# Kernel tuning notes

Measured on AMD Instinct MI355X. Metric: run time of the kernel, lower is better.

The kernel has to match this reference:

```python
import jax, jax.numpy as jnp
import numpy as np

B, S, L, F = 4, 4, 1024, 256
D, H = 256, 8
DH = D // H


def setup_inputs() -> dict:
    key = jax.random.key(0)
    ks = jax.random.split(key, 9)
    scale = 0.06  # ~1/sqrt(fan_in) init scale
    return {
        "x": jax.random.normal(ks[0], (B, S, L, F), dtype=jnp.float32),
        "Wq": jax.random.normal(ks[1], (D, F), dtype=jnp.float32) * scale,
        "bq": jnp.zeros((D,), dtype=jnp.float32),
        "Wk": jax.random.normal(ks[2], (D, F), dtype=jnp.float32) * scale,
        "bk": jnp.zeros((D,), dtype=jnp.float32),
        "Wv": jax.random.normal(ks[3], (D, F), dtype=jnp.float32) * scale,
        "bv": jnp.zeros((D,), dtype=jnp.float32),
        "Wo": jax.random.normal(ks[4], (D, D), dtype=jnp.float32) * scale,
        "bo": jnp.zeros((D,), dtype=jnp.float32),
    }


def reference(x, Wq, bq, Wk, bk, Wv, bv, Wo, bo):
    b, s, l, f = x.shape
    xr = x.reshape(b * s, l, f)  # [N, L, F] with N = batch*samples

    def split_heads(t):  # [N, L, D] -> [N, H, L, DH]
        return t.reshape(b * s, l, H, DH).transpose(0, 2, 1, 3)

    q = split_heads(xr @ Wq.T + bq)
    k = split_heads(xr @ Wk.T + bk)
    v = split_heads(xr @ Wv.T + bv)

    scores = jnp.einsum("nhqd,nhkd->nhqk", q, k) / jnp.sqrt(jnp.float32(DH))
    probs = jax.nn.softmax(scores, axis=-1)  # [N, H, L, L] — materialized as in original
    out = jnp.einsum("nhqk,nhkd->nhqd", probs, v)

    out = out.transpose(0, 2, 1, 3).reshape(b * s, l, D)
    out = out @ Wo.T + bo
    out = out.reshape(b, s, l, D)

    # softmax pooling over seq_len (dim=2)
    weight = jax.nn.softmax(out, axis=2)
    return jnp.sum(out * weight, axis=2)  # [B, S, D]
```

## Files before the change

kernel.cpp:

```cpp
#include <hip/hip_runtime.h>
#include <math.h>

#define N_SEQ 16
#define LEN   1024
#define FDIM  256
#define DDIM  256
#define NHEAD 8
#define DHD   32
#define ROWS  (N_SEQ * LEN)
#define QSCALE 0.17677669529663687f
#define QKVN  ((size_t)N_SEQ * NHEAD * LEN * DHD)

typedef __attribute__((ext_vector_type(8))) short bf16x8;
typedef __attribute__((ext_vector_type(4))) float f32x4;

__device__ __forceinline__ unsigned short f2bf(float f) {
    unsigned int u = __float_as_uint(f);
    unsigned int r = u + 0x7fffu + ((u >> 16) & 1u);
    return (unsigned short)(r >> 16);
}

__device__ __forceinline__ void load_lds16(const void* g, void* l) {
    __builtin_amdgcn_global_load_lds(
        (const __attribute__((address_space(1))) unsigned int*)g,
        (__attribute__((address_space(3))) unsigned int*)l, 16, 0, 0);
}

__global__ __launch_bounds__(256) void convert_bf16(
    const float* __restrict__ X,
    const float* __restrict__ Wq, const float* __restrict__ Wk,
    const float* __restrict__ Wv, const float* __restrict__ Wo,
    unsigned short* __restrict__ Xbf, unsigned short* __restrict__ Wbf)
{
    const size_t idx4 = ((size_t)blockIdx.x * 256 + threadIdx.x) * 4;
    const float* src;
    unsigned short* dst;
    if (idx4 < (size_t)ROWS * FDIM) {
        src = X + idx4;
        dst = Xbf + idx4;
    } else {
        const size_t wi = idx4 - (size_t)ROWS * FDIM;
        const int w = (int)(wi >> 16);
        const size_t off = wi & 65535;
        const float* Ws[4] = {Wq, Wk, Wv, Wo};
        src = Ws[w] + off;
        dst = Wbf + wi;
    }
    float4 v = *(const float4*)src;
    ushort4 u;
    u.x = f2bf(v.x); u.y = f2bf(v.y); u.z = f2bf(v.z); u.w = f2bf(v.w);
    *(ushort4*)dst = u;
}

template <int MODE>
__global__ __launch_bounds__(256) void gemm_bf16(
    const unsigned short* __restrict__ Ag, const unsigned short* __restrict__ Bg,
    const float* __restrict__ b0, const float* __restrict__ b1,
    const float* __restrict__ b2,
    unsigned short* __restrict__ OutB,
    float* __restrict__ pmO, float* __restrict__ plO, float* __restrict__ psO)
{
    __shared__ unsigned short As[16 * 512];
    __shared__ unsigned short Bs[16 * 512];

    const int m0 = blockIdx.x * 128;
    const int n0 = blockIdx.y * 128;
    const int tid  = threadIdx.x;
    const int wv   = tid >> 6;
    const int lane = tid & 63;
    const int l15  = lane & 15;
    const int quad = lane >> 4;
    const int wr = (wv & 1) * 64;
    const int wc = (wv >> 1) * 64;

    const int isB = wv >> 1;
    const unsigned short* __restrict__ Mg = isB ? Bg : Ag;
    const int mb0 = isB ? n0 : m0;
    unsigned short* Ms = isB ? Bs : As;
    const int fbase = (wv & 1) * 8;

    f32x4 acc[4][4] = {};

    for (int kt = 0; kt < 4; ++kt) {
        __syncthreads();
        #pragma unroll
        for (int f = 0; f < 8; ++f) {
            const int fi = fbase + f;
            const int i = fi >> 1, ks = fi & 1;
            load_lds16(Mg + (size_t)(mb0 + i*16 + l15) * 256 + kt*64 + ks*32 + quad*8,
                       Ms + fi * 512);
        }
        __syncthreads();
        #pragma unroll
        for (int ks = 0; ks < 2; ++ks) {
            bf16x8 af[4], bfr[4];
            #pragma unroll
            for (int i = 0; i < 4; ++i)
                af[i] = *(const bf16x8*)(&As[((((wv & 1)*4 + i)*2) + ks)*512 + lane*8]);
            #pragma unroll
            for (int j = 0; j < 4; ++j)
                bfr[j] = *(const bf16x8*)(&Bs[((((wv >> 1)*4 + j)*2) + ks)*512 + lane*8]);
            #pragma unroll
            for (int i = 0; i < 4; ++i)
                #pragma unroll
                for (int j = 0; j < 4; ++j)
                    acc[i][j] = __builtin_amdgcn_mfma_f32_16x16x32_bf16(
                        af[i], bfr[j], acc[i][j], 0, 0, 0);
        }
    }

    if (MODE == 0) {
        const int mat = n0 >> 8;
        const float scale = (mat == 0) ? QSCALE : 1.0f;
        const float* __restrict__ bias = (mat == 0) ? b0 : (mat == 1) ? b1 : b2;
        unsigned short* __restrict__ Out = OutB + (size_t)mat * QKVN;
        #pragma unroll
        for (int j = 0; j < 4; ++j) {
            const int c  = n0 + wc + j*16 + l15;
            const int cc = c & 255;
            const int h = cc >> 5, dh = cc & 31;
            const float bv = bias[cc];
            #pragma unroll
            for (int i = 0; i < 4; ++i)
                #pragma unroll
                for (int rr = 0; rr < 4; ++rr) {
                    const int r = m0 + wr + i*16 + quad*4 + rr;
                    const int n = r >> 10, l = r & 1023;
                    Out[(((size_t)(n*NHEAD + h)) * LEN + l) * DHD + dh] =
                        f2bf((acc[i][j][rr] + bv) * scale);
                }
        }
    } else {
        const int n    = blockIdx.x >> 3;
        const int tile = blockIdx.x & 7;
        __shared__ float red[4][64];

        float bv[4];
        #pragma unroll
        for (int j = 0; j < 4; ++j) bv[j] = b0[n0 + wc + j*16 + l15];
        #pragma unroll
        for (int i = 0; i < 4; ++i)
            #pragma unroll
            for (int j = 0; j < 4; ++j)
                #pragma unroll
                for (int rr = 0; rr < 4; ++rr)
                    acc[i][j][rr] += bv[j];

        float M[4];
        #pragma unroll
        for (int j = 0; j < 4; ++j) {
            float m = -1e30f;
            #pragma unroll
            for (int i = 0; i < 4; ++i)
                #pragma unroll
                for (int rr = 0; rr < 4; ++rr) m = fmaxf(m, acc[i][j][rr]);
            m = fmaxf(m, __shfl_xor(m, 16));
            m = fmaxf(m, __shfl_xor(m, 32));
            M[j] = m;
        }
        if (quad == 0) {
            #pragma unroll
            for (int j = 0; j < 4; ++j) red[wv][j*16 + l15] = M[j];
        }
        __syncthreads();
        #pragma unroll
        for (int j = 0; j < 4; ++j)
            M[j] = fmaxf(red[wv][j*16 + l15], red[wv^1][j*16 + l15]);
        __syncthreads();

        float LE[4], SE[4];
        #pragma unroll
        for (int j = 0; j < 4; ++j) {
            float le = 0.f, se = 0.f;
            #pragma unroll
            for (int i = 0; i < 4; ++i)
                #pragma unroll
                for (int rr = 0; rr < 4; ++rr) {
                    const float z = acc[i][j][rr];
                    const float e = __expf(z - M[j]);
                    le += e; se += z * e;
                }
            le += __shfl_xor(le, 16); le += __shfl_xor(le, 32);
            se += __shfl_xor(se, 16); se += __shfl_xor(se, 32);
            LE[j] = le; SE[j] = se;
        }
        if (quad == 0) {
            #pragma unroll
            for (int j = 0; j < 4; ++j) red[wv][j*16 + l15] = LE[j];
        }
        __syncthreads();
        float LEp[4];
        #pragma unroll
        for (int j = 0; j < 4; ++j) LEp[j] = red[wv^1][j*16 + l15];
        __syncthreads();
        if (quad == 0) {
            #pragma unroll
            for (int j = 0; j < 4; ++j) red[wv][j*16 + l15] = SE[j];
        }
        __syncthreads();
        float SEp[4];
        #pragma unroll
        for (int j = 0; j < 4; ++j) SEp[j] = red[wv^1][j*16 + l15];

        if ((wv & 1) == 0 && quad == 0) {
            #pragma unroll
            for (int j = 0; j < 4; ++j) {
                const int c = n0 + wc + j*16 + l15;
                const size_t o = ((size_t)n*8 + tile)*256 + c;
                pmO[o] = M[j];
                plO[o] = LE[j] + LEp[j];
                psO[o] = SE[j] + SEp[j];
            }
        }
    }
}

__global__ __launch_bounds__(256) void vtrans(
    const unsigned short* __restrict__ Vb, unsigned short* __restrict__ Vtb)
{
    __shared__ unsigned short Ls[64 * 34];

    const int nh = blockIdx.y;
    const int l0 = blockIdx.x * 64;
    const int tid = threadIdx.x;

    const int row = tid >> 2, c8 = (tid & 3) * 8;
    *(bf16x8*)(&Ls[row*34 + c8]) =
        *(const bf16x8*)(Vb + ((size_t)nh * LEN + l0 + row) * DHD + c8);
    __syncthreads();

    const int dh = tid >> 3, l8 = (tid & 7) * 8;
    ushort4 u0, u1;
    u0.x = Ls[(l8+0)*34 + dh]; u0.y = Ls[(l8+1)*34 + dh];
    u0.z = Ls[(l8+2)*34 + dh]; u0.w = Ls[(l8+3)*34 + dh];
    u1.x = Ls[(l8+4)*34 + dh]; u1.y = Ls[(l8+5)*34 + dh];
    u1.z = Ls[(l8+6)*34 + dh]; u1.w = Ls[(l8+7)*34 + dh];
    unsigned short* dst = Vtb + ((size_t)nh * DHD + dh) * LEN + l0 + l8;
    *(ushort4*)(dst)     = u0;
    *(ushort4*)(dst + 4) = u1;
}

#define LDK2 40
#define LDV2 136
#define LDPk 72
__global__ __launch_bounds__(256) void attn_mfma(
    const unsigned short* __restrict__ Qg_, const unsigned short* __restrict__ Kg_,
    const unsigned short* __restrict__ Vg_, unsigned short* __restrict__ Aout)
{
    __shared__ unsigned short Ks[128 * LDK2];
    __shared__ unsigned short Vs[32 * LDV2];
    __shared__ unsigned short Pb[4][16 * LDPk];

    const int nh = blockIdx.y;
    const int n  = nh >> 3, h = nh & 7;
    const int q0 = blockIdx.x * 64;
    const int tid  = threadIdx.x;
    const int wv   = tid >> 6;
    const int lane = tid & 63;
    const int l15  = lane & 15;
    const int quad = lane >> 4;

    const unsigned short* __restrict__ Qg = Qg_ + (size_t)nh * LEN * DHD;
    const unsigned short* __restrict__ Kg = Kg_ + (size_t)nh * LEN * DHD;
    const unsigned short* __restrict__ Vg = Vg_ + (size_t)nh * DHD * LEN;

    bf16x8 qf = *(const bf16x8*)(Qg + (size_t)(q0 + wv*16 + l15) * DHD + quad*8);

    f32x4 o0 = {0.f, 0.f, 0.f, 0.f};
    f32x4 o1 = {0.f, 0.f, 0.f, 0.f};
    float l_lane = 0.f;

    const int krow = tid >> 2, kc8 = (tid & 3) * 8;
    const int vrow = tid >> 3, vc8 = (tid & 7) * 8;

    unsigned short* __restrict__ Pw = &Pb[wv][0];

    for (int kt = 0; kt < LEN / 128; ++kt) {
        const int k0 = kt * 128;
        __syncthreads();
        *(bf16x8*)(&Ks[krow*LDK2 + kc8]) =
            *(const bf16x8*)(Kg + (size_t)(k0 + krow)*DHD + kc8);
        *(bf16x8*)(&Ks[(64 + krow)*LDK2 + kc8]) =
            *(const bf16x8*)(Kg + (size_t)(k0 + 64 + krow)*DHD + kc8);
        *(bf16x8*)(&Vs[vrow*LDV2 + vc8]) =
            *(const bf16x8*)(Vg + (size_t)vrow*LEN + k0 + vc8);
        *(bf16x8*)(&Vs[vrow*LDV2 + 64 + vc8]) =
            *(const bf16x8*)(Vg + (size_t)vrow*LEN + k0 + 64 + vc8);
        __syncthreads();

        #pragma unroll
        for (int half = 0; half < 2; ++half) {
            f32x4 st[4];
            #pragma unroll
            for (int sub = 0; sub < 4; ++sub) {
                bf16x8 kf = *(const bf16x8*)(&Ks[(half*64 + sub*16 + l15)*LDK2 + quad*8]);
                f32x4 z = {0.f, 0.f, 0.f, 0.f};
                st[sub] = __builtin_amdgcn_mfma_f32_16x16x32_bf16(kf, qf, z, 0, 0, 0);
            }
            #pragma unroll
            for (int sub = 0; sub < 4; ++sub) {
                const float p0 = __expf(st[sub][0]);
                const float p1 = __expf(st[sub][1]);
                const float p2 = __expf(st[sub][2]);
                const float p3 = __expf(st[sub][3]);
                l_lane += (p0 + p1) + (p2 + p3);
                uint2 pk;
                pk.x = (unsigned int)f2bf(p0) | ((unsigned int)f2bf(p1) << 16);
                pk.y = (unsigned int)f2bf(p2) | ((unsigned int)f2bf(p3) << 16);
                *(uint2*)(&Pw[l15*LDPk + sub*16 + quad*4]) = pk;
            }
            #pragma unroll
            for (int kk = 0; kk < 2; ++kk) {
                bf16x8 pf = *(const bf16x8*)(&Pw[l15*LDPk + kk*32 + quad*8]);
                bf16x8 va = *(const bf16x8*)(&Vs[l15*LDV2 + half*64 + kk*32 + quad*8]);
                bf16x8 vb = *(const bf16x8*)(&Vs[(16 + l15)*LDV2 + half*64 + kk*32 + quad*8]);
                o0 = __builtin_amdgcn_mfma_f32_16x16x32_bf16(va, pf, o0, 0, 0, 0);
                o1 = __builtin_amdgcn_mfma_f32_16x16x32_bf16(vb, pf, o1, 0, 0, 0);
            }
        }
    }

    l_lane += __shfl_xor(l_lane, 16);
    l_lane += __shfl_xor(l_lane, 32);
    const float linv = 1.f / l_lane;

    float* __restrict__ Tw = (float*)&Pb[wv][0];
    #pragma unroll
    for (int r = 0; r < 4; ++r) {
        Tw[l15*36 + quad*4 + r]      = o0[r] * linv;
        Tw[l15*36 + 16 + quad*4 + r] = o1[r] * linv;
    }
    __syncthreads();
    const int qr = lane >> 2, c8 = (lane & 3) * 8;
    float4 r0 = *(const float4*)(&Tw[qr*36 + c8]);
    float4 r1 = *(const float4*)(&Tw[qr*36 + c8 + 4]);
    unsigned short* dst = Aout + ((size_t)(n*LEN + q0 + wv*16 + qr)) * DDIM + h*DHD + c8;
    ushort4 u0, u1;
    u0.x = f2bf(r0.x); u0.y = f2bf(r0.y); u0.z = f2bf(r0.z); u0.w = f2bf(r0.w);
    u1.x = f2bf(r1.x); u1.y = f2bf(r1.y); u1.z = f2bf(r1.z); u1.w = f2bf(r1.w);
    *(ushort4*)(dst)     = u0;
    *(ushort4*)(dst + 4) = u1;
}

__global__ __launch_bounds__(256) void pool_merge(
    const float* __restrict__ pm, const float* __restrict__ pl,
    const float* __restrict__ ps, float* __restrict__ out)
{
    const int n = blockIdx.x;
    const int d = threadIdx.x;
    float M = -1e30f;
    #pragma unroll
    for (int t = 0; t < 8; ++t) M = fmaxf(M, pm[((size_t)n*8 + t)*256 + d]);
    float L = 0.f, S = 0.f;
    #pragma unroll
    for (int t = 0; t < 8; ++t) {
        const size_t idx = ((size_t)n*8 + t)*256 + d;
        const float w = __expf(pm[idx] - M);
        L += pl[idx] * w;
        S += ps[idx] * w;
    }
    out[n*256 + d] = S / L;
}

extern "C" void kernel_launch(void* const* d_in, const int* in_sizes, int n_in,
                              void* d_out, int out_size, void* d_ws, size_t ws_size,
                              hipStream_t stream)
{
    const float* x  = (const float*)d_in[0];
    const float* Wq = (const float*)d_in[1];
    const float* bq = (const float*)d_in[2];
    const float* Wk = (const float*)d_in[3];
    const float* bk = (const float*)d_in[4];
    const float* Wv = (const float*)d_in[5];
    const float* bv = (const float*)d_in[6];
    const float* Wo = (const float*)d_in[7];
    const float* bo = (const float*)d_in[8];
    float* out = (float*)d_out;

    char* base = (char*)d_ws;
    unsigned short* Xbf  = (unsigned short*)(base);
    unsigned short* Qb   = (unsigned short*)(base +  8388608);
    unsigned short* Kb   = (unsigned short*)(base + 16777216);
    unsigned short* Vb   = (unsigned short*)(base + 25165824);
    unsigned short* Vtb  = (unsigned short*)(base + 33554432);
    unsigned short* attnb= (unsigned short*)(base + 41943040);
    unsigned short* Wbf  = (unsigned short*)(base + 50331648);
    float* pm = (float*)(base + 50855936);
    float* pl = (float*)(base + 50987008);
    float* ps = (float*)(base + 51118080);
    const size_t need_bytes = 51249152;
    if (ws_size < need_bytes) return;

    convert_bf16<<<4352, 256, 0, stream>>>(x, Wq, Wk, Wv, Wo, Xbf, Wbf);
    gemm_bf16<0><<<dim3(ROWS/128, 6), 256, 0, stream>>>(
        Xbf, Wbf, bq, bk, bv, Qb, nullptr, nullptr, nullptr);
    vtrans<<<dim3(LEN/64, N_SEQ*NHEAD), 256, 0, stream>>>(Vb, Vtb);
    attn_mfma<<<dim3(LEN/64, N_SEQ*NHEAD), 256, 0, stream>>>(Qb, Kb, Vtb, attnb);
    gemm_bf16<1><<<dim3(ROWS/128, 2), 256, 0, stream>>>(
        attnb, Wbf + (size_t)768*256, bo, nullptr, nullptr, nullptr, pm, pl, ps);
    pool_merge<<<16, 256, 0, stream>>>(pm, pl, ps, out);
}
```

Baseline: 159.8 us.

## Write V in MFMA fragment layout, drop vtrans, stream K/V from registers

The QKV GEMM epilogue now writes V straight into the per-lane MFMA fragment layout, so the separate vtrans transpose kernel is removed. The attention kernel no longer stages K and V through shared memory with block barriers. Each lane loads its K/V fragments from global memory with one-step register prefetch, and each wave handles 64 queries (4 groups), so every K/V load is reused four times. P is now truncated to bf16 rather than rounded, and the row sum uses those same truncated values. This cuts launches and LDS traffic but raises register pressure and reduces the grid to a quarter as many blocks.

```diff
diff --git a/kernel.cpp b/kernel.cpp
--- a/kernel.cpp
+++ b/kernel.cpp
@@ -111,24 +111,52 @@
 
     if (MODE == 0) {
         const int mat = n0 >> 8;
-        const float scale = (mat == 0) ? QSCALE : 1.0f;
-        const float* __restrict__ bias = (mat == 0) ? b0 : (mat == 1) ? b1 : b2;
-        unsigned short* __restrict__ Out = OutB + (size_t)mat * QKVN;
-        #pragma unroll
-        for (int j = 0; j < 4; ++j) {
-            const int c  = n0 + wc + j*16 + l15;
-            const int cc = c & 255;
-            const int h = cc >> 5, dh = cc & 31;
-            const float bv = bias[cc];
-            #pragma unroll
-            for (int i = 0; i < 4; ++i)
-                #pragma unroll
-                for (int rr = 0; rr < 4; ++rr) {
-                    const int r = m0 + wr + i*16 + quad*4 + rr;
-                    const int n = r >> 10, l = r & 1023;
-                    Out[(((size_t)(n*NHEAD + h)) * LEN + l) * DHD + dh] =
-                        f2bf((acc[i][j][rr] + bv) * scale);
+        if (mat != 2) {
+            const float scale = (mat == 0) ? QSCALE : 1.0f;
+            const float* __restrict__ bias = (mat == 0) ? b0 : b1;
+            unsigned short* __restrict__ Out = OutB + (size_t)mat * QKVN;
+            #pragma unroll
+            for (int j = 0; j < 4; ++j) {
+                const int c  = n0 + wc + j*16 + l15;
+                const int cc = c & 255;
+                const int h = cc >> 5, dh = cc & 31;
+                const float bv = bias[cc];
+                #pragma unroll
+                for (int i = 0; i < 4; ++i)
+                    #pragma unroll
+                    for (int rr = 0; rr < 4; ++rr) {
+                        const int r = m0 + wr + i*16 + quad*4 + rr;
+                        const int n = r >> 10, l = r & 1023;
+                        Out[(((size_t)(n*NHEAD + h)) * LEN + l) * DHD + dh] =
+                            f2bf((acc[i][j][rr] + bv) * scale);
+                    }
+            }
+        } else {
+            unsigned short* __restrict__ Vf = OutB + 2 * QKVN;
+            #pragma unroll
+            for (int j = 0; j < 4; ++j) {
+                const int c  = n0 + wc + j*16 + l15;
+                const int cc = c & 255;
+                const int h = cc >> 5, dh = cc & 31;
+                const int dhb = dh >> 4, mv = dh & 15;
+                const float bv = b2[cc];
+                #pragma unroll
+                for (int i = 0; i < 4; ++i) {
+                    const int r0 = m0 + wr + i*16 + quad*4;
+                    const int n = r0 >> 10, l0 = r0 & 1023;
+                    const int nh = n*NHEAD + h;
+                    const int kb = l0 >> 5;
+                    const int qv = (l0 & 31) >> 3, jv0 = l0 & 7;
+                    const size_t addr =
+                        (((size_t)nh*32 + kb)*2 + dhb)*512 + (qv*16 + mv)*8 + jv0;
+                    ushort4 u;
+                    u.x = f2bf(acc[i][j][0] + bv);
+                    u.y = f2bf(acc[i][j][1] + bv);
+                    u.z = f2bf(acc[i][j][2] + bv);
+                    u.w = f2bf(acc[i][j][3] + bv);
+                    *(ushort4*)(Vf + addr) = u;
                 }
+            }
         }
     } else {
         const int n    = blockIdx.x >> 3;
@@ -215,45 +243,16 @@
     }
 }
 
-__global__ __launch_bounds__(256) void vtrans(
-    const unsigned short* __restrict__ Vb, unsigned short* __restrict__ Vtb)
-{
-    __shared__ unsigned short Ls[64 * 34];
-
-    const int nh = blockIdx.y;
-    const int l0 = blockIdx.x * 64;
-    const int tid = threadIdx.x;
-
-    const int row = tid >> 2, c8 = (tid & 3) * 8;
-    *(bf16x8*)(&Ls[row*34 + c8]) =
-        *(const bf16x8*)(Vb + ((size_t)nh * LEN + l0 + row) * DHD + c8);
-    __syncthreads();
-
-    const int dh = tid >> 3, l8 = (tid & 7) * 8;
-    ushort4 u0, u1;
-    u0.x = Ls[(l8+0)*34 + dh]; u0.y = Ls[(l8+1)*34 + dh];
-    u0.z = Ls[(l8+2)*34 + dh]; u0.w = Ls[(l8+3)*34 + dh];
-    u1.x = Ls[(l8+4)*34 + dh]; u1.y = Ls[(l8+5)*34 + dh];
-    u1.z = Ls[(l8+6)*34 + dh]; u1.w = Ls[(l8+7)*34 + dh];
-    unsigned short* dst = Vtb + ((size_t)nh * DHD + dh) * LEN + l0 + l8;
-    *(ushort4*)(dst)     = u0;
-    *(ushort4*)(dst + 4) = u1;
-}
-
-#define LDK2 40
-#define LDV2 136
 #define LDPk 72
 __global__ __launch_bounds__(256) void attn_mfma(
     const unsigned short* __restrict__ Qg_, const unsigned short* __restrict__ Kg_,
-    const unsigned short* __restrict__ Vg_, unsigned short* __restrict__ Aout)
+    const unsigned short* __restrict__ Vf_, unsigned short* __restrict__ Aout)
 {
-    __shared__ unsigned short Ks[128 * LDK2];
-    __shared__ unsigned short Vs[32 * LDV2];
     __shared__ unsigned short Pb[4][16 * LDPk];
 
     const int nh = blockIdx.y;
     const int n  = nh >> 3, h = nh & 7;
-    const int q0 = blockIdx.x * 64;
+    const int q0 = blockIdx.x * 256;
     const int tid  = threadIdx.x;
     const int wv   = tid >> 6;
     const int lane = tid & 63;
@@ -262,84 +261,104 @@
 
     const unsigned short* __restrict__ Qg = Qg_ + (size_t)nh * LEN * DHD;
     const unsigned short* __restrict__ Kg = Kg_ + (size_t)nh * LEN * DHD;
-    const unsigned short* __restrict__ Vg = Vg_ + (size_t)nh * DHD * LEN;
-
-    bf16x8 qf = *(const bf16x8*)(Qg + (size_t)(q0 + wv*16 + l15) * DHD + quad*8);
-
-    f32x4 o0 = {0.f, 0.f, 0.f, 0.f};
-    f32x4 o1 = {0.f, 0.f, 0.f, 0.f};
-    float l_lane = 0.f;
-
-    const int krow = tid >> 2, kc8 = (tid & 3) * 8;
-    const int vrow = tid >> 3, vc8 = (tid & 7) * 8;
+    const unsigned short* __restrict__ Vf = Vf_ + (size_t)nh * 32768;
+
+    bf16x8 qf[4];
+    #pragma unroll
+    for (int g = 0; g < 4; ++g)
+        qf[g] = *(const bf16x8*)(Qg + (size_t)(q0 + wv*64 + g*16 + l15) * DHD + quad*8);
+
+    f32x4 oA[4] = {{0.f,0.f,0.f,0.f},{0.f,0.f,0.f,0.f},{0.f,0.f,0.f,0.f},{0.f,0.f,0.f,0.f}};
+    f32x4 oB[4] = {{0.f,0.f,0.f,0.f},{0.f,0.f,0.f,0.f},{0.f,0.f,0.f,0.f},{0.f,0.f,0.f,0.f}};
+    float l_acc[4] = {0.f, 0.f, 0.f, 0.f};
+
+    const unsigned short* __restrict__ kbase = Kg + (size_t)l15 * DHD + quad*8;
+    const unsigned short* __restrict__ vbase = Vf + lane*8;
+
+    bf16x8 kf[4], vv[4];
+    #pragma unroll
+    for (int s = 0; s < 4; ++s) kf[s] = *(const bf16x8*)(kbase + (size_t)(s*16) * DHD);
+    #pragma unroll
+    for (int j = 0; j < 4; ++j) vv[j] = *(const bf16x8*)(vbase + j*512);
 
     unsigned short* __restrict__ Pw = &Pb[wv][0];
 
-    for (int kt = 0; kt < LEN / 128; ++kt) {
-        const int k0 = kt * 128;
-        __syncthreads();
-        *(bf16x8*)(&Ks[krow*LDK2 + kc8]) =
-            *(const bf16x8*)(Kg + (size_t)(k0 + krow)*DHD + kc8);
-        *(bf16x8*)(&Ks[(64 + krow)*LDK2 + kc8]) =
-            *(const bf16x8*)(Kg + (size_t)(k0 + 64 + krow)*DHD + kc8);
-        *(bf16x8*)(&Vs[vrow*LDV2 + vc8]) =
-            *(const bf16x8*)(Vg + (size_t)vrow*LEN + k0 + vc8);
-        *(bf16x8*)(&Vs[vrow*LDV2 + 64 + vc8]) =
-            *(const bf16x8*)(Vg + (size_t)vrow*LEN + k0 + 64 + vc8);
-        __syncthreads();
-
-        #pragma unroll
-        for (int half = 0; half < 2; ++half) {
+    for (int t = 0; t < 16; ++t) {
+        bf16x8 kn[4], vn[4];
+        if (t < 15) {
+            #pragma unroll
+            for (int s = 0; s < 4; ++s)
+                kn[s] = *(const bf16x8*)(kbase + (size_t)((t+1)*64 + s*16) * DHD);
+            #pragma unroll
+            for (int j = 0; j < 4; ++j)
+                vn[j] = *(const bf16x8*)(vbase + ((t+1)*4 + j)*512);
+        }
+        #pragma unroll
+        for (int g = 0; g < 4; ++g) {
             f32x4 st[4];
             #pragma unroll
-            for (int sub = 0; sub < 4; ++sub) {
-                bf16x8 kf = *(const bf16x8*)(&Ks[(half*64 + sub*16 + l15)*LDK2 + quad*8]);
+            for (int s = 0; s < 4; ++s) {
                 f32x4 z = {0.f, 0.f, 0.f, 0.f};
-                st[sub] = __builtin_amdgcn_mfma_f32_16x16x32_bf16(kf, qf, z, 0, 0, 0);
-            }
-            #pragma unroll
-            for (int sub = 0; sub < 4; ++sub) {
-                const float p0 = __expf(st[sub][0]);
-                const float p1 = __expf(st[sub][1]);
-                const float p2 = __expf(st[sub][2]);
-                const float p3 = __expf(st[sub][3]);
-                l_lane += (p0 + p1) + (p2 + p3);
+                st[s] = __builtin_amdgcn_mfma_f32_16x16x32_bf16(kf[s], qf[g], z, 0, 0, 0);
+            }
+            float lg = 0.f;
+            #pragma unroll
+            for (int s = 0; s < 4; ++s) {
+                const unsigned int a0 = __float_as_uint(__expf(st[s][0])) & 0xffff0000u;
+                const unsigned int a1 = __float_as_uint(__expf(st[s][1])) & 0xffff0000u;
+                const unsigned int a2 = __float_as_uint(__expf(st[s][2])) & 0xffff0000u;
+                const unsigned int a3 = __float_as_uint(__expf(st[s][3])) & 0xffff0000u;
+                lg += (__uint_as_float(a0) + __uint_as_float(a1))
+                    + (__uint_as_float(a2) + __uint_as_float(a3));
                 uint2 pk;
-                pk.x = (unsigned int)f2bf(p0) | ((unsigned int)f2bf(p1) << 16);
-                pk.y = (unsigned int)f2bf(p2) | ((unsigned int)f2bf(p3) << 16);
-                *(uint2*)(&Pw[l15*LDPk + sub*16 + quad*4]) = pk;
-            }
+                pk.x = (a0 >> 16) | a1;
+                pk.y = (a2 >> 16) | a3;
+                *(uint2*)(&Pw[l15*LDPk + s*16 + quad*4]) = pk;
+            }
+            l_acc[g] += lg;
             #pragma unroll
             for (int kk = 0; kk < 2; ++kk) {
                 bf16x8 pf = *(const bf16x8*)(&Pw[l15*LDPk + kk*32 + quad*8]);
-                bf16x8 va = *(const bf16x8*)(&Vs[l15*LDV2 + half*64 + kk*32 + quad*8]);
-                bf16x8 vb = *(const bf16x8*)(&Vs[(16 + l15)*LDV2 + half*64 + kk*32 + quad*8]);
-                o0 = __builtin_amdgcn_mfma_f32_16x16x32_bf16(va, pf, o0, 0, 0, 0);
-                o1 = __builtin_amdgcn_mfma_f32_16x16x32_bf16(vb, pf, o1, 0, 0, 0);
-            }
-        }
-    }
-
-    l_lane += __shfl_xor(l_lane, 16);
-    l_lane += __shfl_xor(l_lane, 32);
-    const float linv = 1.f / l_lane;
+                oA[g] = __builtin_amdgcn_mfma_f32_16x16x32_bf16(vv[kk*2+0], pf, oA[g], 0, 0, 0);
+                oB[g] = __builtin_amdgcn_mfma_f32_16x16x32_bf16(vv[kk*2+1], pf, oB[g], 0, 0, 0);
+            }
+        }
+        if (t < 15) {
+            #pragma unroll
+            for (int s = 0; s < 4; ++s) kf[s] = kn[s];
+            #pragma unroll
+            for (int j = 0; j < 4; ++j) vv[j] = vn[j];
+        }
+    }
+
+    float linv[4];
+    #pragma unroll
+    for (int g = 0; g < 4; ++g) {
+        float tsum = l_acc[g];
+        tsum += __shfl_xor(tsum, 16);
+        tsum += __shfl_xor(tsum, 32);
+        linv[g] = 1.f / tsum;
+    }
 
     float* __restrict__ Tw = (float*)&Pb[wv][0];
-    #pragma unroll
-    for (int r = 0; r < 4; ++r) {
-        Tw[l15*36 + quad*4 + r]      = o0[r] * linv;
-        Tw[l15*36 + 16 + quad*4 + r] = o1[r] * linv;
-    }
-    __syncthreads();
     const int qr = lane >> 2, c8 = (lane & 3) * 8;
-    float4 r0 = *(const float4*)(&Tw[qr*36 + c8]);
-    float4 r1 = *(const float4*)(&Tw[qr*36 + c8 + 4]);
-    unsigned short* dst = Aout + ((size_t)(n*LEN + q0 + wv*16 + qr)) * DDIM + h*DHD + c8;
-    ushort4 u0, u1;
-    u0.x = f2bf(r0.x); u0.y = f2bf(r0.y); u0.z = f2bf(r0.z); u0.w = f2bf(r0.w);
-    u1.x = f2bf(r1.x); u1.y = f2bf(r1.y); u1.z = f2bf(r1.z); u1.w = f2bf(r1.w);
-    *(ushort4*)(dst)     = u0;
-    *(ushort4*)(dst + 4) = u1;
+    #pragma unroll
+    for (int g = 0; g < 4; ++g) {
+        #pragma unroll
+        for (int r = 0; r < 4; ++r) {
+            Tw[l15*36 + quad*4 + r]      = oA[g][r] * linv[g];
+            Tw[l15*36 + 16 + quad*4 + r] = oB[g][r] * linv[g];
+        }
+        float4 r0 = *(const float4*)(&Tw[qr*36 + c8]);
+        float4 r1 = *(const float4*)(&Tw[qr*36 + c8 + 4]);
+        unsigned short* dst =
+            Aout + ((size_t)(n*LEN + q0 + wv*64 + g*16 + qr)) * DDIM + h*DHD + c8;
+        ushort4 u0, u1;
+        u0.x = f2bf(r0.x); u0.y = f2bf(r0.y); u0.z = f2bf(r0.z); u0.w = f2bf(r0.w);
+        u1.x = f2bf(r1.x); u1.y = f2bf(r1.y); u1.z = f2bf(r1.z); u1.w = f2bf(r1.w);
+        *(ushort4*)(dst)     = u0;
+        *(ushort4*)(dst + 4) = u1;
+    }
 }
 
 __global__ __launch_bounds__(256) void pool_merge(
@@ -380,9 +399,7 @@
     char* base = (char*)d_ws;
     unsigned short* Xbf  = (unsigned short*)(base);
     unsigned short* Qb   = (unsigned short*)(base +  8388608);
-    unsigned short* Kb   = (unsigned short*)(base + 16777216);
-    unsigned short* Vb   = (unsigned short*)(base + 25165824);
-    unsigned short* Vtb  = (unsigned short*)(base + 33554432);
+    unsigned short* Vfrag= (unsigned short*)(base + 25165824);
     unsigned short* attnb= (unsigned short*)(base + 41943040);
     unsigned short* Wbf  = (unsigned short*)(base + 50331648);
     float* pm = (float*)(base + 50855936);
@@ -394,8 +411,8 @@
     convert_bf16<<<4352, 256, 0, stream>>>(x, Wq, Wk, Wv, Wo, Xbf, Wbf);
     gemm_bf16<0><<<dim3(ROWS/128, 6), 256, 0, stream>>>(
         Xbf, Wbf, bq, bk, bv, Qb, nullptr, nullptr, nullptr);
-    vtrans<<<dim3(LEN/64, N_SEQ*NHEAD), 256, 0, stream>>>(Vb, Vtb);
-    attn_mfma<<<dim3(LEN/64, N_SEQ*NHEAD), 256, 0, stream>>>(Qb, Kb, Vtb, attnb);
+    attn_mfma<<<dim3(LEN/256, N_SEQ*NHEAD), 256, 0, stream>>>(
+        Qb, Qb + QKVN, Vfrag, attnb);
     gemm_bf16<1><<<dim3(ROWS/128, 2), 256, 0, stream>>>(
         attnb, Wbf + (size_t)768*256, bo, nullptr, nullptr, nullptr, pm, pl, ps);
     pool_merge<<<16, 256, 0, stream>>>(pm, pl, ps, out);
```

Measured after the change: 140.8 us. -11.9%, faster.
